# Optimization experiments

Measured on AMD Instinct MI355X. Metric: run time of the kernel, lower is better.

Reference implementation:

```python
import jax, jax.numpy as jnp
import numpy as np


def setup_inputs() -> dict:
    key = jax.random.key(0)
    k1, k2 = jax.random.split(key)
    B, T, D, K = 8, 4096, 256, 1024
    z = jax.random.normal(k1, (B, T, D), dtype=jnp.float32)
    codebook = jax.random.uniform(k2, (K, D), dtype=jnp.float32)
    return {"z": z, "codebook": codebook}


def reference(z, codebook):
    # Squared L2 distance via dot-product decomposition (same argmin as
    # the broadcasted squared-difference in the original module, without
    # materializing the (B,T,K,D) intermediate).
    #   ||z - c||^2 = ||z||^2 - 2 z.c + ||c||^2
    z_sq = jnp.sum(z * z, axis=-1, keepdims=True)            # (B,T,1)
    c_sq = jnp.sum(codebook * codebook, axis=-1)             # (K,)
    cross = jnp.einsum("btd,kd->btk", z, codebook)           # (B,T,K)
    l2_distance = z_sq - 2.0 * cross + c_sq                  # (B,T,K)
    codebook_indices = jnp.argmin(l2_distance, axis=-1)      # (B,T)
    z_q = codebook[codebook_indices]                         # (B,T,D)
    # Straight-through estimator
    z_q = z + jax.lax.stop_gradient(z_q - z)
    return (z_q, codebook_indices)
```

## Files before the change

kernel.cpp:

```cpp
#include <hip/hip_runtime.h>
#include <math.h>

#define NTOK   32768
#define NDIM   256
#define NCODE  1024

#define TM 128
#define TN 128
#define KC 32
#define NTILES (NCODE / TN)

typedef _Float16 f16x8 __attribute__((ext_vector_type(8)));
typedef _Float16 f16x4 __attribute__((ext_vector_type(4)));
typedef float    f32x4 __attribute__((ext_vector_type(4)));

__device__ __forceinline__ void gld_lds16(const void* g, void* l) {
    __builtin_amdgcn_global_load_lds(
        (const __attribute__((address_space(1))) void*)g,
        (__attribute__((address_space(3))) void*)l, 16, 0, 0);
}

__global__ __launch_bounds__(256) void split_z(const float* __restrict__ z,
                                               _Float16* __restrict__ zh,
                                               _Float16* __restrict__ zl) {
    size_t i = ((size_t)blockIdx.x * 256 + threadIdx.x) * 8;
    float4 a0 = *(const float4*)(z + i);
    float4 a1 = *(const float4*)(z + i + 4);
    float v[8] = {a0.x, a0.y, a0.z, a0.w, a1.x, a1.y, a1.z, a1.w};
    f16x8 hi, lo;
    #pragma unroll
    for (int e = 0; e < 8; ++e) {
        _Float16 h = (_Float16)v[e];
        hi[e] = h;
        lo[e] = (_Float16)(v[e] - (float)h);
    }
    *(f16x8*)&zh[i] = hi;
    *(f16x8*)&zl[i] = lo;
}

__global__ __launch_bounds__(256) void split_cb(const float* __restrict__ cb,
                                                _Float16* __restrict__ ch,
                                                _Float16* __restrict__ cl,
                                                float* __restrict__ csq) {
    int row  = blockIdx.x * 4 + (threadIdx.x >> 6);
    int lane = threadIdx.x & 63;
    const float* src = cb + (size_t)row * NDIM + lane * 4;
    float4 v = *(const float4*)src;
    float s = v.x * v.x + v.y * v.y + v.z * v.z + v.w * v.w;
    float a[4] = {v.x, v.y, v.z, v.w};
    f16x4 hi, lo;
    #pragma unroll
    for (int e = 0; e < 4; ++e) {
        _Float16 h = (_Float16)a[e];
        hi[e] = h;
        lo[e] = (_Float16)(a[e] - (float)h);
    }
    *(f16x4*)&ch[(size_t)row * NDIM + lane * 4] = hi;
    *(f16x4*)&cl[(size_t)row * NDIM + lane * 4] = lo;
    #pragma unroll
    for (int off = 32; off > 0; off >>= 1) s += __shfl_down(s, off, 64);
    if (lane == 0) csq[row] = s;
}

__global__ __launch_bounds__(256, 3) void vq_mfma_argmin(
        const _Float16* __restrict__ zh, const _Float16* __restrict__ zl,
        const _Float16* __restrict__ ch, const _Float16* __restrict__ cl,
        const float* __restrict__ csq,
        float* __restrict__ pv, int* __restrict__ pi) {
    __shared__ _Float16 Ah[TM * KC];
    __shared__ _Float16 Al[TM * KC];
    __shared__ _Float16 Bh[TN * KC];
    __shared__ _Float16 Bl[TN * KC];

    const int tid    = threadIdx.x;
    const int nstrip = blockIdx.x;
    const int m0     = blockIdx.y * TM;
    const int n0     = nstrip * TN;
    const int wave   = tid >> 6;
    const int lane   = tid & 63;
    const int wy = wave >> 1, wx = wave & 1;
    const int quad = lane >> 4, lr = lane & 15;

    const _Float16* gsrc;
    _Float16* ldst;
    if      (wave == 0) { gsrc = zh + (size_t)m0 * NDIM; ldst = Ah; }
    else if (wave == 1) { gsrc = zl + (size_t)m0 * NDIM; ldst = Al; }
    else if (wave == 2) { gsrc = ch + (size_t)n0 * NDIM; ldst = Bh; }
    else                { gsrc = cl + (size_t)n0 * NDIM; ldst = Bl; }
    gsrc += (lane >> 2) * NDIM + (lane & 3) * 8;

    f32x4 acc[4][4];
    #pragma unroll
    for (int i = 0; i < 4; ++i)
        #pragma unroll
        for (int j = 0; j < 4; ++j) acc[i][j] = (f32x4){0.f, 0.f, 0.f, 0.f};

    for (int kc = 0; kc < NDIM; kc += KC) {
        __syncthreads();
        #pragma unroll
        for (int j = 0; j < 8; ++j)
            gld_lds16(gsrc + kc + j * 16 * NDIM, ldst + j * 512);
        __syncthreads();

        f16x8 fah[4], fal[4], fbh[4], fbl[4];
        #pragma unroll
        for (int t = 0; t < 4; ++t) {
            int aoff = (wy * 64 + t * 16 + lr) * KC + quad * 8;
            int boff = (wx * 64 + t * 16 + lr) * KC + quad * 8;
            fah[t] = *(const f16x8*)&Ah[aoff];
            fal[t] = *(const f16x8*)&Al[aoff];
            fbh[t] = *(const f16x8*)&Bh[boff];
            fbl[t] = *(const f16x8*)&Bl[boff];
        }
        #pragma unroll
        for (int mt = 0; mt < 4; ++mt)
            #pragma unroll
            for (int nt = 0; nt < 4; ++nt) {
                acc[mt][nt] = __builtin_amdgcn_mfma_f32_16x16x32_f16(
                                  fah[mt], fbh[nt], acc[mt][nt], 0, 0, 0);
                acc[mt][nt] = __builtin_amdgcn_mfma_f32_16x16x32_f16(
                                  fal[mt], fbh[nt], acc[mt][nt], 0, 0, 0);
                acc[mt][nt] = __builtin_amdgcn_mfma_f32_16x16x32_f16(
                                  fah[mt], fbl[nt], acc[mt][nt], 0, 0, 0);
            }
    }

    float cs[4];
    #pragma unroll
    for (int nt = 0; nt < 4; ++nt) cs[nt] = csq[n0 + wx * 64 + nt * 16 + lr];

    __syncthreads();
    float* cv = (float*)Ah;
    int*   ci = (int*)Bh;

    #pragma unroll
    for (int mt = 0; mt < 4; ++mt)
        #pragma unroll
        for (int r = 0; r < 4; ++r) {
            float bv = INFINITY; int bi = 0x7fffffff;
            #pragma unroll
            for (int nt = 0; nt < 4; ++nt) {
                float v = cs[nt] - 2.0f * acc[mt][nt][r];
                int   n = n0 + wx * 64 + nt * 16 + lr;
                if (v < bv || (v == bv && n < bi)) { bv = v; bi = n; }
            }
            #pragma unroll
            for (int msk = 1; msk < 16; msk <<= 1) {
                float ov = __shfl_xor(bv, msk, 64);
                int   oi = __shfl_xor(bi, msk, 64);
                if (ov < bv || (ov == bv && oi < bi)) { bv = ov; bi = oi; }
            }
            if (lr == 0) {
                int ml = wy * 64 + mt * 16 + quad * 4 + r;
                cv[ml * 2 + wx] = bv;
                ci[ml * 2 + wx] = bi;
            }
        }
    __syncthreads();

    if (tid < TM) {
        float v0 = cv[tid * 2], v1 = cv[tid * 2 + 1];
        int   i0 = ci[tid * 2], i1 = ci[tid * 2 + 1];
        bool take1 = (v1 < v0) || (v1 == v0 && i1 < i0);
        int token = m0 + tid;
        pv[token * NTILES + nstrip] = take1 ? v1 : v0;
        pi[token * NTILES + nstrip] = take1 ? i1 : i0;
    }
}

__global__ __launch_bounds__(256) void vq_finalize(
        const float* __restrict__ pv, const int* __restrict__ pi,
        const float* __restrict__ cb,
        float* __restrict__ zq, float* __restrict__ io) {
    __shared__ int best[16];
    const int tid = threadIdx.x;
    const int t0 = blockIdx.x * 16;

    if (tid < 16) {
        int token = t0 + tid;
        float bv = INFINITY; int bi = 0x7fffffff;
        #pragma unroll
        for (int j = 0; j < NTILES; ++j) {
            float v = pv[token * NTILES + j];
            int   i = pi[token * NTILES + j];
            if (v < bv || (v == bv && i < bi)) { bv = v; bi = i; }
        }
        best[tid] = bi;
        io[token] = (float)bi;
    }
    __syncthreads();

    const int tr = tid >> 4, tc = tid & 15;
    const float* src = cb + (size_t)best[tr] * NDIM;
    float*       dst = zq + (size_t)(t0 + tr) * NDIM;
    #pragma unroll
    for (int q = 0; q < 4; ++q) {
        int col = q * 64 + tc * 4;
        *(float4*)&dst[col] = *(const float4*)&src[col];
    }
}

extern "C" void kernel_launch(void* const* d_in, const int* in_sizes, int n_in,
                              void* d_out, int out_size, void* d_ws, size_t ws_size,
                              hipStream_t stream) {
    const float* z  = (const float*)d_in[0];
    const float* cb = (const float*)d_in[1];

    float* zq = (float*)d_out;
    float* io = (float*)d_out + (size_t)NTOK * NDIM;

    _Float16* zh = (_Float16*)d_out;
    _Float16* zl = zh + (size_t)NTOK * NDIM;

    _Float16* ch  = (_Float16*)d_ws;
    _Float16* cl  = ch + (size_t)NCODE * NDIM;
    float*    csq = (float*)(cl + (size_t)NCODE * NDIM);
    float*    pv  = csq + NCODE;
    int*      pi  = (int*)(pv + (size_t)NTOK * NTILES);

    split_z<<<NTOK * NDIM / (256 * 8), 256, 0, stream>>>(z, zh, zl);
    split_cb<<<NCODE / 4, 256, 0, stream>>>(cb, ch, cl, csq);

    dim3 grid(NTILES, NTOK / TM);
    vq_mfma_argmin<<<grid, 256, 0, stream>>>(zh, zl, ch, cl, csq, pv, pi);

    vq_finalize<<<NTOK / 16, 256, 0, stream>>>(pv, pi, cb, zq, io);
}
```

Before: 163.3 us.

## Pre-tile fp16 split operands, merge prep kernels, pack partial argmin pairs

Combines the z and codebook split kernels into one launch. That launch writes the hi/lo fp16 halves in a chunked tile-major layout (128 rows x 32 k contiguous), so each wave's global-to-LDS loads become fully contiguous 1 KB streams instead of strided row segments. Partial argmin results are packed as float2 (value, index bits), which halves the number of scattered stores and loads. The MFMA kernel's launch-bounds occupancy hint rises from 3 to 4 blocks per CU, which may constrain register allocation.

```diff
diff --git a/kernel.cpp b/kernel.cpp
--- a/kernel.cpp
+++ b/kernel.cpp
@@ -9,9 +9,9 @@
 #define TN 128
 #define KC 32
 #define NTILES (NCODE / TN)
+#define CHUNK  (128 * KC)
 
 typedef _Float16 f16x8 __attribute__((ext_vector_type(8)));
-typedef _Float16 f16x4 __attribute__((ext_vector_type(4)));
 typedef float    f32x4 __attribute__((ext_vector_type(4)));
 
 __device__ __forceinline__ void gld_lds16(const void* g, void* l) {
@@ -20,53 +20,49 @@
         (__attribute__((address_space(3))) void*)l, 16, 0, 0);
 }
 
-__global__ __launch_bounds__(256) void split_z(const float* __restrict__ z,
-                                               _Float16* __restrict__ zh,
-                                               _Float16* __restrict__ zl) {
-    size_t i = ((size_t)blockIdx.x * 256 + threadIdx.x) * 8;
-    float4 a0 = *(const float4*)(z + i);
-    float4 a1 = *(const float4*)(z + i + 4);
+__global__ __launch_bounds__(256) void prep_split(
+        const float* __restrict__ z, const float* __restrict__ cb,
+        _Float16* __restrict__ zh, _Float16* __restrict__ zl,
+        _Float16* __restrict__ ch, _Float16* __restrict__ cl,
+        float* __restrict__ csq) {
+    const bool is_cb = blockIdx.x >= 4096;
+    const int  bb    = is_cb ? (blockIdx.x - 4096) : blockIdx.x;
+    const int  L     = bb * 256 + threadIdx.x;
+    const int  row   = L >> 5;
+    const int  g     = L & 31;
+
+    const float* src = (is_cb ? cb : z) + (size_t)row * NDIM + g * 8;
+    float4 a0 = *(const float4*)src;
+    float4 a1 = *(const float4*)(src + 4);
     float v[8] = {a0.x, a0.y, a0.z, a0.w, a1.x, a1.y, a1.z, a1.w};
     f16x8 hi, lo;
+    float s = 0.f;
     #pragma unroll
     for (int e = 0; e < 8; ++e) {
         _Float16 h = (_Float16)v[e];
         hi[e] = h;
         lo[e] = (_Float16)(v[e] - (float)h);
-    }
-    *(f16x8*)&zh[i] = hi;
-    *(f16x8*)&zl[i] = lo;
-}
-
-__global__ __launch_bounds__(256) void split_cb(const float* __restrict__ cb,
-                                                _Float16* __restrict__ ch,
-                                                _Float16* __restrict__ cl,
-                                                float* __restrict__ csq) {
-    int row  = blockIdx.x * 4 + (threadIdx.x >> 6);
-    int lane = threadIdx.x & 63;
-    const float* src = cb + (size_t)row * NDIM + lane * 4;
-    float4 v = *(const float4*)src;
-    float s = v.x * v.x + v.y * v.y + v.z * v.z + v.w * v.w;
-    float a[4] = {v.x, v.y, v.z, v.w};
-    f16x4 hi, lo;
-    #pragma unroll
-    for (int e = 0; e < 4; ++e) {
-        _Float16 h = (_Float16)a[e];
-        hi[e] = h;
-        lo[e] = (_Float16)(a[e] - (float)h);
-    }
-    *(f16x4*)&ch[(size_t)row * NDIM + lane * 4] = hi;
-    *(f16x4*)&cl[(size_t)row * NDIM + lane * 4] = lo;
-    #pragma unroll
-    for (int off = 32; off > 0; off >>= 1) s += __shfl_down(s, off, 64);
-    if (lane == 0) csq[row] = s;
-}
-
-__global__ __launch_bounds__(256, 3) void vq_mfma_argmin(
+        s += v[e] * v[e];
+    }
+    const int rb = row >> 7, r = row & 127, kc8 = g >> 2, k8 = g & 3;
+    const size_t dst = (size_t)(rb * 8 + kc8) * CHUNK + r * KC + k8 * 8;
+    if (is_cb) {
+        *(f16x8*)&ch[dst] = hi;
+        *(f16x8*)&cl[dst] = lo;
+        #pragma unroll
+        for (int off = 16; off > 0; off >>= 1) s += __shfl_down(s, off, 32);
+        if ((threadIdx.x & 31) == 0) csq[row] = s;
+    } else {
+        *(f16x8*)&zh[dst] = hi;
+        *(f16x8*)&zl[dst] = lo;
+    }
+}
+
+__global__ __launch_bounds__(256, 4) void vq_mfma_argmin(
         const _Float16* __restrict__ zh, const _Float16* __restrict__ zl,
         const _Float16* __restrict__ ch, const _Float16* __restrict__ cl,
         const float* __restrict__ csq,
-        float* __restrict__ pv, int* __restrict__ pi) {
+        float2* __restrict__ pq) {
     __shared__ _Float16 Ah[TM * KC];
     __shared__ _Float16 Al[TM * KC];
     __shared__ _Float16 Bh[TN * KC];
@@ -74,7 +70,7 @@
 
     const int tid    = threadIdx.x;
     const int nstrip = blockIdx.x;
-    const int m0     = blockIdx.y * TM;
+    const int mblk   = blockIdx.y;
     const int n0     = nstrip * TN;
     const int wave   = tid >> 6;
     const int lane   = tid & 63;
@@ -83,11 +79,11 @@
 
     const _Float16* gsrc;
     _Float16* ldst;
-    if      (wave == 0) { gsrc = zh + (size_t)m0 * NDIM; ldst = Ah; }
-    else if (wave == 1) { gsrc = zl + (size_t)m0 * NDIM; ldst = Al; }
-    else if (wave == 2) { gsrc = ch + (size_t)n0 * NDIM; ldst = Bh; }
-    else                { gsrc = cl + (size_t)n0 * NDIM; ldst = Bl; }
-    gsrc += (lane >> 2) * NDIM + (lane & 3) * 8;
+    if      (wave == 0) { gsrc = zh + (size_t)mblk * (8 * CHUNK); ldst = Ah; }
+    else if (wave == 1) { gsrc = zl + (size_t)mblk * (8 * CHUNK); ldst = Al; }
+    else if (wave == 2) { gsrc = ch + (size_t)nstrip * (8 * CHUNK); ldst = Bh; }
+    else                { gsrc = cl + (size_t)nstrip * (8 * CHUNK); ldst = Bl; }
+    gsrc += lane * 8;
 
     f32x4 acc[4][4];
     #pragma unroll
@@ -95,11 +91,11 @@
         #pragma unroll
         for (int j = 0; j < 4; ++j) acc[i][j] = (f32x4){0.f, 0.f, 0.f, 0.f};
 
-    for (int kc = 0; kc < NDIM; kc += KC) {
+    for (int kc8 = 0; kc8 < 8; ++kc8) {
         __syncthreads();
         #pragma unroll
         for (int j = 0; j < 8; ++j)
-            gld_lds16(gsrc + kc + j * 16 * NDIM, ldst + j * 512);
+            gld_lds16(gsrc + kc8 * CHUNK + j * 512, ldst + j * 512);
         __syncthreads();
 
         f16x8 fah[4], fal[4], fbh[4], fbl[4];
@@ -162,15 +158,14 @@
         float v0 = cv[tid * 2], v1 = cv[tid * 2 + 1];
         int   i0 = ci[tid * 2], i1 = ci[tid * 2 + 1];
         bool take1 = (v1 < v0) || (v1 == v0 && i1 < i0);
-        int token = m0 + tid;
-        pv[token * NTILES + nstrip] = take1 ? v1 : v0;
-        pi[token * NTILES + nstrip] = take1 ? i1 : i0;
+        int token = mblk * TM + tid;
+        pq[(size_t)token * NTILES + nstrip] =
+            make_float2(take1 ? v1 : v0, __int_as_float(take1 ? i1 : i0));
     }
 }
 
 __global__ __launch_bounds__(256) void vq_finalize(
-        const float* __restrict__ pv, const int* __restrict__ pi,
-        const float* __restrict__ cb,
+        const float2* __restrict__ pq, const float* __restrict__ cb,
         float* __restrict__ zq, float* __restrict__ io) {
     __shared__ int best[16];
     const int tid = threadIdx.x;
@@ -181,9 +176,9 @@
         float bv = INFINITY; int bi = 0x7fffffff;
         #pragma unroll
         for (int j = 0; j < NTILES; ++j) {
-            float v = pv[token * NTILES + j];
-            int   i = pi[token * NTILES + j];
-            if (v < bv || (v == bv && i < bi)) { bv = v; bi = i; }
+            float2 p = pq[(size_t)token * NTILES + j];
+            int i = __float_as_int(p.y);
+            if (p.x < bv || (p.x == bv && i < bi)) { bv = p.x; bi = i; }
         }
         best[tid] = bi;
         io[token] = (float)bi;
@@ -215,14 +210,12 @@
     _Float16* ch  = (_Float16*)d_ws;
     _Float16* cl  = ch + (size_t)NCODE * NDIM;
     float*    csq = (float*)(cl + (size_t)NCODE * NDIM);
-    float*    pv  = csq + NCODE;
-    int*      pi  = (int*)(pv + (size_t)NTOK * NTILES);
-
-    split_z<<<NTOK * NDIM / (256 * 8), 256, 0, stream>>>(z, zh, zl);
-    split_cb<<<NCODE / 4, 256, 0, stream>>>(cb, ch, cl, csq);
+    float2*   pq  = (float2*)(csq + NCODE);
+
+    prep_split<<<4096 + 128, 256, 0, stream>>>(z, cb, zh, zl, ch, cl, csq);
 
     dim3 grid(NTILES, NTOK / TM);
-    vq_mfma_argmin<<<grid, 256, 0, stream>>>(zh, zl, ch, cl, csq, pv, pi);
-
-    vq_finalize<<<NTOK / 16, 256, 0, stream>>>(pv, pi, cb, zq, io);
-}
+    vq_mfma_argmin<<<grid, 256, 0, stream>>>(zh, zl, ch, cl, csq, pq);
+
+    vq_finalize<<<NTOK / 16, 256, 0, stream>>>(pq, cb, zq, io);
+}
```

Result: faster. 158.1 us (-3.2%).
